# Performance work log

Hardware: AMD Instinct MI355X
Metric: run time of the kernel (lower is better)

The kernel has to match this reference:

```python
import jax, jax.numpy as jnp
import numpy as np

N = 100000
E = 1600000
F_IN = 128
HID = 64


def setup_inputs() -> dict:
    key = jax.random.key(0)
    ks = jax.random.split(key, 8)
    x = jax.random.normal(ks[0], (N, F_IN), dtype=jnp.float32)
    edge_index = jax.random.randint(ks[1], (2, E), 0, N, dtype=jnp.int32)
    # GCNConv params: weight [in, out] (glorot-ish scale), bias [out]
    W1 = jax.random.normal(ks[2], (F_IN, HID), dtype=jnp.float32) / np.sqrt(F_IN)
    b1 = jnp.zeros((HID,), dtype=jnp.float32)
    W2 = jax.random.normal(ks[3], (HID, HID), dtype=jnp.float32) / np.sqrt(HID)
    b2 = jnp.zeros((HID,), dtype=jnp.float32)
    Wc = jax.random.normal(ks[4], (HID, 1), dtype=jnp.float32) / np.sqrt(HID)
    bc = jnp.zeros((1,), dtype=jnp.float32)
    return {"x": x, "edge_index": edge_index, "W1": W1, "b1": b1,
            "W2": W2, "b2": b2, "Wc": Wc, "bc": bc}


def _gcn_conv(x, src, dst, W, b):
    # PyG GCNConv: h = x @ W, then symmetric-normalized aggregation over
    # edges with self-loops: out[d] = sum_e deg^-1/2[s] deg^-1/2[d] h[s] + b
    n = x.shape[0]
    h = x @ W                                            # [N, out]
    deg = jax.ops.segment_sum(jnp.ones_like(dst, dtype=h.dtype), dst,
                              num_segments=n)            # in-degree incl. self-loops
    dinv = jnp.where(deg > 0, jax.lax.rsqrt(deg), 0.0)   # [N]
    norm = dinv[src] * dinv[dst]                         # [E+N]
    msg = h[src] * norm[:, None]                         # gather + scale
    out = jax.ops.segment_sum(msg, dst, num_segments=n)  # scatter-add
    return out + b


def reference(x, edge_index, W1, b1, W2, b2, Wc, bc):
    n = x.shape[0]
    loop = jnp.arange(n, dtype=edge_index.dtype)
    src = jnp.concatenate([edge_index[0], loop])  # add self-loops
    dst = jnp.concatenate([edge_index[1], loop])
    h = jax.nn.relu(_gcn_conv(x, src, dst, W1, b1))  # dropout in eval mode = identity
    h = jax.nn.relu(_gcn_conv(h, src, dst, W2, b2))
    return (h @ Wc + bc).squeeze(-1)  # [N]
```

## Files before the change

kernel.cpp:

```cpp
#include <hip/hip_runtime.h>


#define FIN 128
#define HIDDEN 64
#define BUCK_SH 7
#define BUCK_MASK 127
#define NBUCK 782
#define CAP 2432
#define EPB 2048

typedef __attribute__((ext_vector_type(8))) short bf16x8;
typedef __attribute__((ext_vector_type(4))) float f32x4;

__device__ __forceinline__ unsigned f2bf_pair(float a, float b) {
    unsigned ua = __float_as_uint(a);
    unsigned ub = __float_as_uint(b);
    ua = (ua + 0x7FFFu + ((ua >> 16) & 1u)) >> 16;
    ub = (ub + 0x7FFFu + ((ub >> 16) & 1u)) & 0xFFFF0000u;
    return ua | ub;
}
__device__ __forceinline__ unsigned short f2bf1(float a) {
    unsigned u = __float_as_uint(a);
    return (unsigned short)((u + 0x7FFFu + ((u >> 16) & 1u)) >> 16);
}
#define BF_LO(u) __uint_as_float((u) << 16)
#define BF_HI(u) __uint_as_float((u) & 0xFFFF0000u)

__global__ __launch_bounds__(256) void k_prep(const float* __restrict__ w1,
                                              const float* __restrict__ w2,
                                              unsigned short* __restrict__ w1t,
                                              unsigned short* __restrict__ w2t,
                                              int* __restrict__ bcursor) {
    int t = blockIdx.x * 256 + threadIdx.x;
    if (t < NBUCK) bcursor[t] = 0;
    for (int i = t; i < 64 * FIN; i += 16384) {
        int ch = i >> 7, k = i & 127;
        w1t[i] = f2bf1(w1[k * 64 + ch]);
    }
    if (t < 64 * 64) {
        int ch = t >> 6, k = t & 63;
        w2t[t] = f2bf1(w2[k * 64 + ch]);
    }
}

__global__ __launch_bounds__(256) void k_scatter_mfma1(const int* __restrict__ src,
                                                       const int* __restrict__ dst,
                                                       int* __restrict__ bcursor,
                                                       int* __restrict__ pairs, int e,
                                                       const float4* __restrict__ x4,
                                                       const unsigned short* __restrict__ w1t,
                                                       uint2* __restrict__ hsb,
                                                       int n, int nsc, int ngm) {
    __shared__ int sbuf[4352];
    int tid = threadIdx.x;
    int bid = blockIdx.x;
    bool is_sc = (bid & 1) == 0;
    int id = bid >> 1;
    if (is_sc) {
        if (id >= nsc) return;
        int* h      = sbuf;
        int* base_s = sbuf + NBUCK;
        int* cur    = sbuf + 2 * NBUCK;
        int dloc[EPB / 256];
        for (int i = tid; i < NBUCK; i += 256) { h[i] = 0; cur[i] = 0; }
        __syncthreads();
        int start = id * EPB;
#pragma unroll
        for (int i = 0; i < EPB / 256; i++) {
            int idx = start + tid + i * 256;
            int d = (idx < e) ? dst[idx] : -1;
            dloc[i] = d;
            if (d >= 0) atomicAdd(&h[d >> BUCK_SH], 1);
        }
        __syncthreads();
        for (int i = tid; i < NBUCK; i += 256)
            if (h[i] > 0) base_s[i] = atomicAdd(&bcursor[i], h[i]);
        __syncthreads();
#pragma unroll
        for (int i = 0; i < EPB / 256; i++) {
            int idx = start + tid + i * 256;
            int d = dloc[i];
            if (d >= 0) {
                int b = d >> BUCK_SH;
                int pos = base_s[b] + atomicAdd(&cur[b], 1);
                if (pos < CAP) pairs[b * CAP + pos] = (src[idx] << BUCK_SH) | (d & BUCK_MASK);
            }
        }
        return;
    }
    if (id >= ngm) return;
    unsigned short* sW = (unsigned short*)sbuf;
    {
        int ch = tid >> 2, k0 = (tid & 3) * 32;
        const uint4* g = (const uint4*)(w1t + ch * 128 + k0);
        uint4* dsd = (uint4*)(sW + ch * 136 + k0);
        uint4 a = g[0], b = g[1], c = g[2], d = g[3];
        dsd[0] = a; dsd[1] = b; dsd[2] = c; dsd[3] = d;
    }
    __syncthreads();
    int lane = tid & 63, wave = tid >> 6;
    int quad = lane >> 4, nl = lane & 15;
    const bf16x8* sW8 = (const bf16x8*)sW;
    int node0g = id * 128;
#pragma unroll
    for (int hf = 0; hf < 2; hf++) {
        int node = node0g + hf * 64 + wave * 16 + nl;
        int ic = min(node, n - 1);
        const float4* px = x4 + (size_t)ic * 32 + quad * 2;
        bf16x8 bfr[4];
#pragma unroll
        for (int kc = 0; kc < 4; kc++) {
            float4 p = px[kc * 8];
            float4 q = px[kc * 8 + 1];
            union { unsigned u[4]; bf16x8 v; } t;
            t.u[0] = f2bf_pair(p.x, p.y); t.u[1] = f2bf_pair(p.z, p.w);
            t.u[2] = f2bf_pair(q.x, q.y); t.u[3] = f2bf_pair(q.z, q.w);
            bfr[kc] = t.v;
        }
        f32x4 a0 = {0.f, 0.f, 0.f, 0.f}, a1 = a0, a2 = a0, a3 = a0;
#pragma unroll
        for (int kc = 0; kc < 4; kc++) {
            int ko = kc * 4 + quad;
            bf16x8 w0  = sW8[(nl +  0) * 17 + ko];
            bf16x8 w1f = sW8[(nl + 16) * 17 + ko];
            bf16x8 w2f = sW8[(nl + 32) * 17 + ko];
            bf16x8 w3f = sW8[(nl + 48) * 17 + ko];
            a0 = __builtin_amdgcn_mfma_f32_16x16x32_bf16(w0,  bfr[kc], a0, 0, 0, 0);
            a1 = __builtin_amdgcn_mfma_f32_16x16x32_bf16(w1f, bfr[kc], a1, 0, 0, 0);
            a2 = __builtin_amdgcn_mfma_f32_16x16x32_bf16(w2f, bfr[kc], a2, 0, 0, 0);
            a3 = __builtin_amdgcn_mfma_f32_16x16x32_bf16(w3f, bfr[kc], a3, 0, 0, 0);
        }
        if (node < n) {
            uint2* o = hsb + (size_t)node * 16 + quad;
            o[0]  = make_uint2(f2bf_pair(a0.x, a0.y), f2bf_pair(a0.z, a0.w));
            o[4]  = make_uint2(f2bf_pair(a1.x, a1.y), f2bf_pair(a1.z, a1.w));
            o[8]  = make_uint2(f2bf_pair(a2.x, a2.y), f2bf_pair(a2.z, a2.w));
            o[12] = make_uint2(f2bf_pair(a3.x, a3.y), f2bf_pair(a3.z, a3.w));
        }
    }
}

__global__ __launch_bounds__(256) void k_count(const int* __restrict__ pairs,
                                               const int* __restrict__ bcursor,
                                               float* __restrict__ dinv, int n) {
    __shared__ int cnt[128];
    int tid = threadIdx.x, b = blockIdx.x;
    if (tid < 128) cnt[tid] = 0;
    __syncthreads();
    int c = min(bcursor[b], CAP);
    const int* pb = pairs + b * CAP;
    for (int i = tid; i < c; i += 256) atomicAdd(&cnt[pb[i] & BUCK_MASK], 1);
    __syncthreads();
    int node = (b << BUCK_SH) + tid;
    if (tid < 128 && node < n) dinv[node] = rsqrtf((float)cnt[tid] + 1.0f);
}

__global__ __launch_bounds__(256) void k_agg1_gemm2(const int* __restrict__ pairs,
                                                    const int* __restrict__ bcursor,
                                                    const float* __restrict__ dinv,
                                                    const uint4* __restrict__ hsb4,
                                                    const float4* __restrict__ b1_4,
                                                    const unsigned short* __restrict__ w2t,
                                                    uint2* __restrict__ hsb2, int n) {
    __shared__ int csr_l[CAP];
    __shared__ unsigned short sW[64 * 72];
    __shared__ float sV[32 * 68];
    __shared__ int cnt[128], off_s[128], wsum[128];
    int tid = threadIdx.x, b = blockIdx.x;
    int node0 = b << BUCK_SH;
    if (tid < 128) {
        int ch = tid >> 1, k0 = (tid & 1) * 32;
        const uint4* g = (const uint4*)(w2t + ch * 64 + k0);
        uint4* dsd = (uint4*)(sW + ch * 72 + k0);
        uint4 a = g[0], bb = g[1], c = g[2], d = g[3];
        dsd[0] = a; dsd[1] = bb; dsd[2] = c; dsd[3] = d;
    } else {
        cnt[tid - 128] = 0;
    }
    __syncthreads();
    int c = min(bcursor[b], CAP);
    const int* pb = pairs + b * CAP;
    for (int i = tid; i < c; i += 256) atomicAdd(&cnt[pb[i] & BUCK_MASK], 1);
    __syncthreads();
    if (tid < 128) wsum[tid] = cnt[tid];
    __syncthreads();
    for (int o = 1; o < 128; o <<= 1) {
        int x = 0;
        if (tid < 128 && tid >= o) x = wsum[tid - o];
        __syncthreads();
        if (tid < 128 && tid >= o) wsum[tid] += x;
        __syncthreads();
    }
    if (tid < 128) { off_s[tid] = wsum[tid] - cnt[tid]; cnt[tid] = 0; }
    __syncthreads();
    for (int i = tid; i < c; i += 256) {
        int p = pb[i];
        int l = p & BUCK_MASK;
        int pos = off_s[l] + atomicAdd(&cnt[l], 1);
        csr_l[pos] = p >> BUCK_SH;
    }
    __syncthreads();
    int nloc = tid >> 3, cq = tid & 7;
    int lane = tid & 63, wave = tid >> 6;
    int quad = lane >> 4, nl = lane & 15;
    const bf16x8* sW8 = (const bf16x8*)sW;
#pragma unroll 1
    for (int ck = 0; ck < 4; ck++) {
        int loc = ck * 32 + nloc;
        int node = node0 + loc;
        int dg = cnt[loc], st = off_s[loc];
        float sd = rsqrtf((float)dg + 1.0f);
        float4 accA = make_float4(0.f, 0.f, 0.f, 0.f), accB = accA;
        if (node < n) {
            int end = st + dg;
            int nr = (dg + 3) >> 2;
            for (int r = 0; r < nr; r++) {
                int base = st + (r << 2);
                int e0 = base, e1 = base + 1, e2 = base + 2, e3 = base + 3;
                int s0 = csr_l[min(e0, end - 1)];
                int s1 = csr_l[min(e1, end - 1)];
                int s2 = csr_l[min(e2, end - 1)];
                int s3 = csr_l[min(e3, end - 1)];
                float m0 = (e0 < end) ? dinv[s0] : 0.f;
                float m1 = (e1 < end) ? dinv[s1] : 0.f;
                float m2 = (e2 < end) ? dinv[s2] : 0.f;
                float m3 = (e3 < end) ? dinv[s3] : 0.f;
                uint4 g0 = hsb4[(size_t)s0 * 8 + cq];
                uint4 g1 = hsb4[(size_t)s1 * 8 + cq];
                uint4 g2 = hsb4[(size_t)s2 * 8 + cq];
                uint4 g3 = hsb4[(size_t)s3 * 8 + cq];
                accA.x += m0 * BF_LO(g0.x) + m1 * BF_LO(g1.x) + m2 * BF_LO(g2.x) + m3 * BF_LO(g3.x);
                accA.y += m0 * BF_HI(g0.x) + m1 * BF_HI(g1.x) + m2 * BF_HI(g2.x) + m3 * BF_HI(g3.x);
                accA.z += m0 * BF_LO(g0.y) + m1 * BF_LO(g1.y) + m2 * BF_LO(g2.y) + m3 * BF_LO(g3.y);
                accA.w += m0 * BF_HI(g0.y) + m1 * BF_HI(g1.y) + m2 * BF_HI(g2.y) + m3 * BF_HI(g3.y);
                accB.x += m0 * BF_LO(g0.z) + m1 * BF_LO(g1.z) + m2 * BF_LO(g2.z) + m3 * BF_LO(g3.z);
                accB.y += m0 * BF_HI(g0.z) + m1 * BF_HI(g1.z) + m2 * BF_HI(g2.z) + m3 * BF_HI(g3.z);
                accB.z += m0 * BF_LO(g0.w) + m1 * BF_LO(g1.w) + m2 * BF_LO(g2.w) + m3 * BF_LO(g3.w);
                accB.w += m0 * BF_HI(g0.w) + m1 * BF_HI(g1.w) + m2 * BF_HI(g2.w) + m3 * BF_HI(g3.w);
            }
        }
        float4 vA = make_float4(0.f, 0.f, 0.f, 0.f), vB = vA;
        if (node < n) {
            uint4 gs = hsb4[(size_t)node * 8 + cq];
            float sq = sd * sd;
            float4 bA = b1_4[cq * 2], bB = b1_4[cq * 2 + 1];
            vA.x = fmaxf(sd * accA.x + sq * BF_LO(gs.x) + bA.x, 0.f);
            vA.y = fmaxf(sd * accA.y + sq * BF_HI(gs.x) + bA.y, 0.f);
            vA.z = fmaxf(sd * accA.z + sq * BF_LO(gs.y) + bA.z, 0.f);
            vA.w = fmaxf(sd * accA.w + sq * BF_HI(gs.y) + bA.w, 0.f);
            vB.x = fmaxf(sd * accB.x + sq * BF_LO(gs.z) + bB.x, 0.f);
            vB.y = fmaxf(sd * accB.y + sq * BF_HI(gs.z) + bB.y, 0.f);
            vB.z = fmaxf(sd * accB.z + sq * BF_LO(gs.w) + bB.z, 0.f);
            vB.w = fmaxf(sd * accB.w + sq * BF_HI(gs.w) + bB.w, 0.f);
        }
        float* vb = sV + nloc * 68 + cq * 8;
        *(float4*)vb = vA;
        *(float4*)(vb + 4) = vB;
        __syncthreads();
#pragma unroll
        for (int tt = 0; tt < 2; tt++) {
            f32x4 acc = {0.f, 0.f, 0.f, 0.f};
#pragma unroll
            for (int kc = 0; kc < 2; kc++) {
                const float* vr = sV + (tt * 16 + nl) * 68 + kc * 32 + quad * 8;
                float4 p = *(const float4*)vr;
                float4 q = *(const float4*)(vr + 4);
                union { unsigned u[4]; bf16x8 v; } t;
                t.u[0] = f2bf_pair(p.x, p.y); t.u[1] = f2bf_pair(p.z, p.w);
                t.u[2] = f2bf_pair(q.x, q.y); t.u[3] = f2bf_pair(q.z, q.w);
                bf16x8 a = sW8[(wave * 16 + nl) * 9 + kc * 4 + quad];
                acc = __builtin_amdgcn_mfma_f32_16x16x32_bf16(a, t.v, acc, 0, 0, 0);
            }
            int oloc = ck * 32 + tt * 16 + nl;
            int onode = node0 + oloc;
            if (onode < n) {
                float s = rsqrtf((float)cnt[oloc] + 1.0f);
                hsb2[(size_t)onode * 16 + wave * 4 + quad] =
                    make_uint2(f2bf_pair(acc.x * s, acc.y * s), f2bf_pair(acc.z * s, acc.w * s));
            }
        }
        __syncthreads();
    }
}

__global__ __launch_bounds__(256) void k_agg2_head(const int* __restrict__ pairs,
                                                   const int* __restrict__ bcursor,
                                                   const uint4* __restrict__ hsb4,
                                                   const float4* __restrict__ b2_4,
                                                   const float4* __restrict__ wc_4,
                                                   const float* __restrict__ bc,
                                                   float* __restrict__ out, int n) {
    __shared__ int csr_l[CAP];
    __shared__ int cnt[128], off_s[128], wsum[128];
    int tid = threadIdx.x, b = blockIdx.x;
    int node0 = b << BUCK_SH;
    if (tid < 128) cnt[tid] = 0;
    __syncthreads();
    int c = min(bcursor[b], CAP);
    const int* pb = pairs + b * CAP;
    for (int i = tid; i < c; i += 256) atomicAdd(&cnt[pb[i] & BUCK_MASK], 1);
    __syncthreads();
    if (tid < 128) wsum[tid] = cnt[tid];
    __syncthreads();
    for (int o = 1; o < 128; o <<= 1) {
        int x = 0;
        if (tid < 128 && tid >= o) x = wsum[tid - o];
        __syncthreads();
        if (tid < 128 && tid >= o) wsum[tid] += x;
        __syncthreads();
    }
    if (tid < 128) { off_s[tid] = wsum[tid] - cnt[tid]; cnt[tid] = 0; }
    __syncthreads();
    for (int i = tid; i < c; i += 256) {
        int p = pb[i];
        int l = p & BUCK_MASK;
        int pos = off_s[l] + atomicAdd(&cnt[l], 1);
        csr_l[pos] = p >> BUCK_SH;
    }
    __syncthreads();
    int nloc = tid >> 3, cq = tid & 7;
#pragma unroll 1
    for (int ck = 0; ck < 4; ck++) {
        int loc = ck * 32 + nloc;
        int node = node0 + loc;
        if (node >= n) continue;
        int dg = cnt[loc], st = off_s[loc];
        int end = st + dg;
        float4 accA = make_float4(0.f, 0.f, 0.f, 0.f), accB = accA;
        int nr = (dg + 3) >> 2;
        for (int r = 0; r < nr; r++) {
            int base = st + (r << 2);
            int e0 = base, e1 = base + 1, e2 = base + 2, e3 = base + 3;
            int s0 = csr_l[min(e0, end - 1)];
            int s1 = csr_l[min(e1, end - 1)];
            int s2 = csr_l[min(e2, end - 1)];
            int s3 = csr_l[min(e3, end - 1)];
            float m0 = (e0 < end) ? 1.f : 0.f;
            float m1 = (e1 < end) ? 1.f : 0.f;
            float m2 = (e2 < end) ? 1.f : 0.f;
            float m3 = (e3 < end) ? 1.f : 0.f;
            uint4 g0 = hsb4[(size_t)s0 * 8 + cq];
            uint4 g1 = hsb4[(size_t)s1 * 8 + cq];
            uint4 g2 = hsb4[(size_t)s2 * 8 + cq];
            uint4 g3 = hsb4[(size_t)s3 * 8 + cq];
            accA.x += m0 * BF_LO(g0.x) + m1 * BF_LO(g1.x) + m2 * BF_LO(g2.x) + m3 * BF_LO(g3.x);
            accA.y += m0 * BF_HI(g0.x) + m1 * BF_HI(g1.x) + m2 * BF_HI(g2.x) + m3 * BF_HI(g3.x);
            accA.z += m0 * BF_LO(g0.y) + m1 * BF_LO(g1.y) + m2 * BF_LO(g2.y) + m3 * BF_LO(g3.y);
            accA.w += m0 * BF_HI(g0.y) + m1 * BF_HI(g1.y) + m2 * BF_HI(g2.y) + m3 * BF_HI(g3.y);
            accB.x += m0 * BF_LO(g0.z) + m1 * BF_LO(g1.z) + m2 * BF_LO(g2.z) + m3 * BF_LO(g3.z);
            accB.y += m0 * BF_HI(g0.z) + m1 * BF_HI(g1.z) + m2 * BF_HI(g2.z) + m3 * BF_HI(g3.z);
            accB.z += m0 * BF_LO(g0.w) + m1 * BF_LO(g1.w) + m2 * BF_LO(g2.w) + m3 * BF_LO(g3.w);
            accB.w += m0 * BF_HI(g0.w) + m1 * BF_HI(g1.w) + m2 * BF_HI(g2.w) + m3 * BF_HI(g3.w);
        }
        uint4 g = hsb4[(size_t)node * 8 + cq];
        float s = rsqrtf((float)dg + 1.0f);
        float4 bA = b2_4[cq * 2], bB = b2_4[cq * 2 + 1];
        float4 wA = wc_4[cq * 2], wB = wc_4[cq * 2 + 1];
        float t = fmaxf(s * (accA.x + BF_LO(g.x)) + bA.x, 0.f) * wA.x
                + fmaxf(s * (accA.y + BF_HI(g.x)) + bA.y, 0.f) * wA.y
                + fmaxf(s * (accA.z + BF_LO(g.y)) + bA.z, 0.f) * wA.z
                + fmaxf(s * (accA.w + BF_HI(g.y)) + bA.w, 0.f) * wA.w
                + fmaxf(s * (accB.x + BF_LO(g.z)) + bB.x, 0.f) * wB.x
                + fmaxf(s * (accB.y + BF_HI(g.z)) + bB.y, 0.f) * wB.y
                + fmaxf(s * (accB.z + BF_LO(g.w)) + bB.z, 0.f) * wB.z
                + fmaxf(s * (accB.w + BF_HI(g.w)) + bB.w, 0.f) * wB.w;
        t += __shfl_xor(t, 1);
        t += __shfl_xor(t, 2);
        t += __shfl_xor(t, 4);
        if (cq == 0) out[node] = t + bc[0];
    }
}

extern "C" void kernel_launch(void* const* d_in, const int* in_sizes, int n_in,
                              void* d_out, int out_size, void* d_ws, size_t ws_size,
                              hipStream_t stream) {
    const float* x  = (const float*)d_in[0];
    const int*   ei = (const int*)d_in[1];
    const float* W1 = (const float*)d_in[2];
    const float* b1 = (const float*)d_in[3];
    const float* W2 = (const float*)d_in[4];
    const float* b2 = (const float*)d_in[5];
    const float* Wc = (const float*)d_in[6];
    const float* bc = (const float*)d_in[7];
    int n = in_sizes[0] / FIN;
    int e = in_sizes[1] / 2;
    const int* srcv = ei;
    const int* dstv = ei + e;

    char* ws = (char*)d_ws;
    float* dinv    = (float*)(ws + 0);
    int*   bcursor = (int*)(ws + (512u << 10));
    unsigned short* w1t = (unsigned short*)(ws + (528u << 10));
    unsigned short* w2t = (unsigned short*)(ws + (548u << 10));
    int*   pairs   = (int*)(ws + (1u << 20));
    uint2* hsb1    = (uint2*)(ws + (9u << 20));
    uint2* hsb2    = (uint2*)(ws + (22u << 20));

    int nb_sc   = (e + EPB - 1) / EPB;
    int nb_rows = (n + 127) / 128;
    int nb_max  = max(nb_sc, nb_rows);

    k_prep<<<64, 256, 0, stream>>>(W1, W2, w1t, w2t, bcursor);
    k_scatter_mfma1<<<2 * nb_max, 256, 0, stream>>>(srcv, dstv, bcursor, pairs, e,
                                                    (const float4*)x, w1t, hsb1,
                                                    n, nb_sc, nb_rows);
    k_count<<<NBUCK, 256, 0, stream>>>(pairs, bcursor, dinv, n);
    k_agg1_gemm2<<<NBUCK, 256, 0, stream>>>(pairs, bcursor, dinv, (const uint4*)hsb1,
                                            (const float4*)b1, w2t, hsb2, n);
    k_agg2_head<<<NBUCK, 256, 0, stream>>>(pairs, bcursor, (const uint4*)hsb2,
                                           (const float4*)b2, (const float4*)Wc,
                                           bc, (float*)d_out, n);
}
```

Before: 218.2 us.

## Interleave two nodes per gather loop and retile scatter/GEMM block layout

The aggregation loops in both layer kernels now handle two destination nodes per thread group at once, issuing eight independent gathers per iteration instead of four. The goal is more memory-level parallelism on the latency-bound random gathers. The scatter kernel now handles twice as many edges per block, and its scatter and GEMM blocks are laid out contiguously rather than interleaved by parity, which removes idle early-exit blocks. The cost is higher register pressure, wasted work when the two paired nodes have uneven degrees, and padding writes to csr_l so out-of-range reads stay safe.

Result: faster. 212.1 us (-2.8%).

```diff
diff --git a/kernel.cpp b/kernel.cpp
--- a/kernel.cpp
+++ b/kernel.cpp
@@ -7,7 +7,7 @@
 #define BUCK_MASK 127
 #define NBUCK 782
 #define CAP 2432
-#define EPB 2048
+#define EPB 4096
 
 typedef __attribute__((ext_vector_type(8))) short bf16x8;
 typedef __attribute__((ext_vector_type(4))) float f32x4;
@@ -50,14 +50,12 @@
                                                        const float4* __restrict__ x4,
                                                        const unsigned short* __restrict__ w1t,
                                                        uint2* __restrict__ hsb,
-                                                       int n, int nsc, int ngm) {
+                                                       int n, int nsc) {
     __shared__ int sbuf[4352];
     int tid = threadIdx.x;
     int bid = blockIdx.x;
-    bool is_sc = (bid & 1) == 0;
-    int id = bid >> 1;
-    if (is_sc) {
-        if (id >= nsc) return;
+    if (bid < nsc) {
+        int id = bid;
         int* h      = sbuf;
         int* base_s = sbuf + NBUCK;
         int* cur    = sbuf + 2 * NBUCK;
@@ -88,7 +86,7 @@
         }
         return;
     }
-    if (id >= ngm) return;
+    int id = bid - nsc;
     unsigned short* sW = (unsigned short*)sbuf;
     {
         int ch = tid >> 2, k0 = (tid & 3) * 32;
@@ -172,8 +170,8 @@
         int ch = tid >> 1, k0 = (tid & 1) * 32;
         const uint4* g = (const uint4*)(w2t + ch * 64 + k0);
         uint4* dsd = (uint4*)(sW + ch * 72 + k0);
-        uint4 a = g[0], bb = g[1], c = g[2], d = g[3];
-        dsd[0] = a; dsd[1] = bb; dsd[2] = c; dsd[3] = d;
+        uint4 a = g[0], bb = g[1], c2 = g[2], d = g[3];
+        dsd[0] = a; dsd[1] = bb; dsd[2] = c2; dsd[3] = d;
     } else {
         cnt[tid - 128] = 0;
     }
@@ -199,87 +197,99 @@
         int pos = off_s[l] + atomicAdd(&cnt[l], 1);
         csr_l[pos] = p >> BUCK_SH;
     }
+    if (c + tid < CAP) csr_l[c + tid] = 0;
     __syncthreads();
     int nloc = tid >> 3, cq = tid & 7;
     int lane = tid & 63, wave = tid >> 6;
     int quad = lane >> 4, nl = lane & 15;
     const bf16x8* sW8 = (const bf16x8*)sW;
 #pragma unroll 1
-    for (int ck = 0; ck < 4; ck++) {
-        int loc = ck * 32 + nloc;
-        int node = node0 + loc;
-        int dg = cnt[loc], st = off_s[loc];
-        float sd = rsqrtf((float)dg + 1.0f);
-        float4 accA = make_float4(0.f, 0.f, 0.f, 0.f), accB = accA;
-        if (node < n) {
-            int end = st + dg;
-            int nr = (dg + 3) >> 2;
-            for (int r = 0; r < nr; r++) {
-                int base = st + (r << 2);
-                int e0 = base, e1 = base + 1, e2 = base + 2, e3 = base + 3;
-                int s0 = csr_l[min(e0, end - 1)];
-                int s1 = csr_l[min(e1, end - 1)];
-                int s2 = csr_l[min(e2, end - 1)];
-                int s3 = csr_l[min(e3, end - 1)];
-                float m0 = (e0 < end) ? dinv[s0] : 0.f;
-                float m1 = (e1 < end) ? dinv[s1] : 0.f;
-                float m2 = (e2 < end) ? dinv[s2] : 0.f;
-                float m3 = (e3 < end) ? dinv[s3] : 0.f;
-                uint4 g0 = hsb4[(size_t)s0 * 8 + cq];
-                uint4 g1 = hsb4[(size_t)s1 * 8 + cq];
-                uint4 g2 = hsb4[(size_t)s2 * 8 + cq];
-                uint4 g3 = hsb4[(size_t)s3 * 8 + cq];
-                accA.x += m0 * BF_LO(g0.x) + m1 * BF_LO(g1.x) + m2 * BF_LO(g2.x) + m3 * BF_LO(g3.x);
-                accA.y += m0 * BF_HI(g0.x) + m1 * BF_HI(g1.x) + m2 * BF_HI(g2.x) + m3 * BF_HI(g3.x);
-                accA.z += m0 * BF_LO(g0.y) + m1 * BF_LO(g1.y) + m2 * BF_LO(g2.y) + m3 * BF_LO(g3.y);
-                accA.w += m0 * BF_HI(g0.y) + m1 * BF_HI(g1.y) + m2 * BF_HI(g2.y) + m3 * BF_HI(g3.y);
-                accB.x += m0 * BF_LO(g0.z) + m1 * BF_LO(g1.z) + m2 * BF_LO(g2.z) + m3 * BF_LO(g3.z);
-                accB.y += m0 * BF_HI(g0.z) + m1 * BF_HI(g1.z) + m2 * BF_HI(g2.z) + m3 * BF_HI(g3.z);
-                accB.z += m0 * BF_LO(g0.w) + m1 * BF_LO(g1.w) + m2 * BF_LO(g2.w) + m3 * BF_LO(g3.w);
-                accB.w += m0 * BF_HI(g0.w) + m1 * BF_HI(g1.w) + m2 * BF_HI(g2.w) + m3 * BF_HI(g3.w);
+    for (int pk = 0; pk < 2; pk++) {
+        int locA = pk * 64 + nloc, locB = locA + 32;
+        int dgA = cnt[locA], stA = off_s[locA], endA = stA + dgA;
+        int dgB = cnt[locB], stB = off_s[locB], endB = stB + dgB;
+        float4 aAA = make_float4(0.f, 0.f, 0.f, 0.f), aAB = aAA;
+        float4 aBA = aAA, aBB = aAA;
+        int nr = max((dgA + 3) >> 2, (dgB + 3) >> 2);
+        for (int r = 0; r < nr; r++) {
+            int bA = stA + (r << 2), bB = stB + (r << 2);
+            int sA[4], sB[4];
+            float mA[4], mB[4];
+            uint4 gA[4], gB[4];
+#pragma unroll
+            for (int j = 0; j < 4; j++) sA[j] = csr_l[max(min(bA + j, endA - 1), 0)];
+#pragma unroll
+            for (int j = 0; j < 4; j++) sB[j] = csr_l[max(min(bB + j, endB - 1), 0)];
+#pragma unroll
+            for (int j = 0; j < 4; j++) mA[j] = (bA + j < endA) ? dinv[sA[j]] : 0.f;
+#pragma unroll
+            for (int j = 0; j < 4; j++) mB[j] = (bB + j < endB) ? dinv[sB[j]] : 0.f;
+#pragma unroll
+            for (int j = 0; j < 4; j++) gA[j] = hsb4[(size_t)sA[j] * 8 + cq];
+#pragma unroll
+            for (int j = 0; j < 4; j++) gB[j] = hsb4[(size_t)sB[j] * 8 + cq];
+#pragma unroll
+            for (int j = 0; j < 4; j++) {
+                aAA.x += mA[j] * BF_LO(gA[j].x); aAA.y += mA[j] * BF_HI(gA[j].x);
+                aAA.z += mA[j] * BF_LO(gA[j].y); aAA.w += mA[j] * BF_HI(gA[j].y);
+                aAB.x += mA[j] * BF_LO(gA[j].z); aAB.y += mA[j] * BF_HI(gA[j].z);
+                aAB.z += mA[j] * BF_LO(gA[j].w); aAB.w += mA[j] * BF_HI(gA[j].w);
+                aBA.x += mB[j] * BF_LO(gB[j].x); aBA.y += mB[j] * BF_HI(gB[j].x);
+                aBA.z += mB[j] * BF_LO(gB[j].y); aBA.w += mB[j] * BF_HI(gB[j].y);
+                aBB.x += mB[j] * BF_LO(gB[j].z); aBB.y += mB[j] * BF_HI(gB[j].z);
+                aBB.z += mB[j] * BF_LO(gB[j].w); aBB.w += mB[j] * BF_HI(gB[j].w);
             }
         }
-        float4 vA = make_float4(0.f, 0.f, 0.f, 0.f), vB = vA;
-        if (node < n) {
-            uint4 gs = hsb4[(size_t)node * 8 + cq];
-            float sq = sd * sd;
-            float4 bA = b1_4[cq * 2], bB = b1_4[cq * 2 + 1];
-            vA.x = fmaxf(sd * accA.x + sq * BF_LO(gs.x) + bA.x, 0.f);
-            vA.y = fmaxf(sd * accA.y + sq * BF_HI(gs.x) + bA.y, 0.f);
-            vA.z = fmaxf(sd * accA.z + sq * BF_LO(gs.y) + bA.z, 0.f);
-            vA.w = fmaxf(sd * accA.w + sq * BF_HI(gs.y) + bA.w, 0.f);
-            vB.x = fmaxf(sd * accB.x + sq * BF_LO(gs.z) + bB.x, 0.f);
-            vB.y = fmaxf(sd * accB.y + sq * BF_HI(gs.z) + bB.y, 0.f);
-            vB.z = fmaxf(sd * accB.z + sq * BF_LO(gs.w) + bB.z, 0.f);
-            vB.w = fmaxf(sd * accB.w + sq * BF_HI(gs.w) + bB.w, 0.f);
-        }
-        float* vb = sV + nloc * 68 + cq * 8;
-        *(float4*)vb = vA;
-        *(float4*)(vb + 4) = vB;
-        __syncthreads();
-#pragma unroll
-        for (int tt = 0; tt < 2; tt++) {
-            f32x4 acc = {0.f, 0.f, 0.f, 0.f};
-#pragma unroll
-            for (int kc = 0; kc < 2; kc++) {
-                const float* vr = sV + (tt * 16 + nl) * 68 + kc * 32 + quad * 8;
-                float4 p = *(const float4*)vr;
-                float4 q = *(const float4*)(vr + 4);
-                union { unsigned u[4]; bf16x8 v; } t;
-                t.u[0] = f2bf_pair(p.x, p.y); t.u[1] = f2bf_pair(p.z, p.w);
-                t.u[2] = f2bf_pair(q.x, q.y); t.u[3] = f2bf_pair(q.z, q.w);
-                bf16x8 a = sW8[(wave * 16 + nl) * 9 + kc * 4 + quad];
-                acc = __builtin_amdgcn_mfma_f32_16x16x32_bf16(a, t.v, acc, 0, 0, 0);
+#pragma unroll
+        for (int sub = 0; sub < 2; sub++) {
+            int loc = pk * 64 + sub * 32 + nloc;
+            int node = node0 + loc;
+            float4 xA = sub ? aBA : aAA;
+            float4 xB = sub ? aBB : aAB;
+            int dg = sub ? dgB : dgA;
+            float4 vA = make_float4(0.f, 0.f, 0.f, 0.f), vB = vA;
+            if (node < n) {
+                float sd = rsqrtf((float)dg + 1.0f);
+                float sq = sd * sd;
+                uint4 gs = hsb4[(size_t)node * 8 + cq];
+                float4 bA = b1_4[cq * 2], bB = b1_4[cq * 2 + 1];
+                vA.x = fmaxf(sd * xA.x + sq * BF_LO(gs.x) + bA.x, 0.f);
+                vA.y = fmaxf(sd * xA.y + sq * BF_HI(gs.x) + bA.y, 0.f);
+                vA.z = fmaxf(sd * xA.z + sq * BF_LO(gs.y) + bA.z, 0.f);
+                vA.w = fmaxf(sd * xA.w + sq * BF_HI(gs.y) + bA.w, 0.f);
+                vB.x = fmaxf(sd * xB.x + sq * BF_LO(gs.z) + bB.x, 0.f);
+                vB.y = fmaxf(sd * xB.y + sq * BF_HI(gs.z) + bB.y, 0.f);
+                vB.z = fmaxf(sd * xB.z + sq * BF_LO(gs.w) + bB.z, 0.f);
+                vB.w = fmaxf(sd * xB.w + sq * BF_HI(gs.w) + bB.w, 0.f);
             }
-            int oloc = ck * 32 + tt * 16 + nl;
-            int onode = node0 + oloc;
-            if (onode < n) {
-                float s = rsqrtf((float)cnt[oloc] + 1.0f);
-                hsb2[(size_t)onode * 16 + wave * 4 + quad] =
-                    make_uint2(f2bf_pair(acc.x * s, acc.y * s), f2bf_pair(acc.z * s, acc.w * s));
+            float* vb = sV + nloc * 68 + cq * 8;
+            *(float4*)vb = vA;
+            *(float4*)(vb + 4) = vB;
+            __syncthreads();
+#pragma unroll
+            for (int tt = 0; tt < 2; tt++) {
+                f32x4 acc = {0.f, 0.f, 0.f, 0.f};
+#pragma unroll
+                for (int kc = 0; kc < 2; kc++) {
+                    const float* vr = sV + (tt * 16 + nl) * 68 + kc * 32 + quad * 8;
+                    float4 p = *(const float4*)vr;
+                    float4 q = *(const float4*)(vr + 4);
+                    union { unsigned u[4]; bf16x8 v; } t;
+                    t.u[0] = f2bf_pair(p.x, p.y); t.u[1] = f2bf_pair(p.z, p.w);
+                    t.u[2] = f2bf_pair(q.x, q.y); t.u[3] = f2bf_pair(q.z, q.w);
+                    bf16x8 a = sW8[(wave * 16 + nl) * 9 + kc * 4 + quad];
+                    acc = __builtin_amdgcn_mfma_f32_16x16x32_bf16(a, t.v, acc, 0, 0, 0);
+                }
+                int oloc = pk * 64 + sub * 32 + tt * 16 + nl;
+                int onode = node0 + oloc;
+                if (onode < n) {
+                    float s = rsqrtf((float)cnt[oloc] + 1.0f);
+                    hsb2[(size_t)onode * 16 + wave * 4 + quad] =
+                        make_uint2(f2bf_pair(acc.x * s, acc.y * s), f2bf_pair(acc.z * s, acc.w * s));
+                }
             }
-        }
-        __syncthreads();
+            __syncthreads();
+        }
     }
 }
 
@@ -317,57 +327,71 @@
         int pos = off_s[l] + atomicAdd(&cnt[l], 1);
         csr_l[pos] = p >> BUCK_SH;
     }
+    if (c + tid < CAP) csr_l[c + tid] = 0;
     __syncthreads();
     int nloc = tid >> 3, cq = tid & 7;
 #pragma unroll 1
-    for (int ck = 0; ck < 4; ck++) {
-        int loc = ck * 32 + nloc;
-        int node = node0 + loc;
-        if (node >= n) continue;
-        int dg = cnt[loc], st = off_s[loc];
-        int end = st + dg;
-        float4 accA = make_float4(0.f, 0.f, 0.f, 0.f), accB = accA;
-        int nr = (dg + 3) >> 2;
+    for (int pk = 0; pk < 2; pk++) {
+        int locA = pk * 64 + nloc, locB = locA + 32;
+        int dgA = cnt[locA], stA = off_s[locA], endA = stA + dgA;
+        int dgB = cnt[locB], stB = off_s[locB], endB = stB + dgB;
+        float4 aAA = make_float4(0.f, 0.f, 0.f, 0.f), aAB = aAA;
+        float4 aBA = aAA, aBB = aAA;
+        int nr = max((dgA + 3) >> 2, (dgB + 3) >> 2);
         for (int r = 0; r < nr; r++) {
-            int base = st + (r << 2);
-            int e0 = base, e1 = base + 1, e2 = base + 2, e3 = base + 3;
-            int s0 = csr_l[min(e0, end - 1)];
-            int s1 = csr_l[min(e1, end - 1)];
-            int s2 = csr_l[min(e2, end - 1)];
-            int s3 = csr_l[min(e3, end - 1)];
-            float m0 = (e0 < end) ? 1.f : 0.f;
-            float m1 = (e1 < end) ? 1.f : 0.f;
-            float m2 = (e2 < end) ? 1.f : 0.f;
-            float m3 = (e3 < end) ? 1.f : 0.f;
-            uint4 g0 = hsb4[(size_t)s0 * 8 + cq];
-            uint4 g1 = hsb4[(size_t)s1 * 8 + cq];
-            uint4 g2 = hsb4[(size_t)s2 * 8 + cq];
-            uint4 g3 = hsb4[(size_t)s3 * 8 + cq];
-            accA.x += m0 * BF_LO(g0.x) + m1 * BF_LO(g1.x) + m2 * BF_LO(g2.x) + m3 * BF_LO(g3.x);
-            accA.y += m0 * BF_HI(g0.x) + m1 * BF_HI(g1.x) + m2 * BF_HI(g2.x) + m3 * BF_HI(g3.x);
-            accA.z += m0 * BF_LO(g0.y) + m1 * BF_LO(g1.y) + m2 * BF_LO(g2.y) + m3 * BF_LO(g3.y);
-            accA.w += m0 * BF_HI(g0.y) + m1 * BF_HI(g1.y) + m2 * BF_HI(g2.y) + m3 * BF_HI(g3.y);
-            accB.x += m0 * BF_LO(g0.z) + m1 * BF_LO(g1.z) + m2 * BF_LO(g2.z) + m3 * BF_LO(g3.z);
-            accB.y += m0 * BF_HI(g0.z) + m1 * BF_HI(g1.z) + m2 * BF_HI(g2.z) + m3 * BF_HI(g3.z);
-            accB.z += m0 * BF_LO(g0.w) + m1 * BF_LO(g1.w) + m2 * BF_LO(g2.w) + m3 * BF_LO(g3.w);
-            accB.w += m0 * BF_HI(g0.w) + m1 * BF_HI(g1.w) + m2 * BF_HI(g2.w) + m3 * BF_HI(g3.w);
-        }
-        uint4 g = hsb4[(size_t)node * 8 + cq];
-        float s = rsqrtf((float)dg + 1.0f);
-        float4 bA = b2_4[cq * 2], bB = b2_4[cq * 2 + 1];
-        float4 wA = wc_4[cq * 2], wB = wc_4[cq * 2 + 1];
-        float t = fmaxf(s * (accA.x + BF_LO(g.x)) + bA.x, 0.f) * wA.x
-                + fmaxf(s * (accA.y + BF_HI(g.x)) + bA.y, 0.f) * wA.y
-                + fmaxf(s * (accA.z + BF_LO(g.y)) + bA.z, 0.f) * wA.z
-                + fmaxf(s * (accA.w + BF_HI(g.y)) + bA.w, 0.f) * wA.w
-                + fmaxf(s * (accB.x + BF_LO(g.z)) + bB.x, 0.f) * wB.x
-                + fmaxf(s * (accB.y + BF_HI(g.z)) + bB.y, 0.f) * wB.y
-                + fmaxf(s * (accB.z + BF_LO(g.w)) + bB.z, 0.f) * wB.z
-                + fmaxf(s * (accB.w + BF_HI(g.w)) + bB.w, 0.f) * wB.w;
-        t += __shfl_xor(t, 1);
-        t += __shfl_xor(t, 2);
-        t += __shfl_xor(t, 4);
-        if (cq == 0) out[node] = t + bc[0];
+            int bA = stA + (r << 2), bB = stB + (r << 2);
+            int sA[4], sB[4];
+            float mA[4], mB[4];
+            uint4 gA[4], gB[4];
+#pragma unroll
+            for (int j = 0; j < 4; j++) sA[j] = csr_l[max(min(bA + j, endA - 1), 0)];
+#pragma unroll
+            for (int j = 0; j < 4; j++) sB[j] = csr_l[max(min(bB + j, endB - 1), 0)];
+#pragma unroll
+            for (int j = 0; j < 4; j++) mA[j] = (bA + j < endA) ? 1.f : 0.f;
+#pragma unroll
+            for (int j = 0; j < 4; j++) mB[j] = (bB + j < endB) ? 1.f : 0.f;
+#pragma unroll
+            for (int j = 0; j < 4; j++) gA[j] = hsb4[(size_t)sA[j] * 8 + cq];
+#pragma unroll
+            for (int j = 0; j < 4; j++) gB[j] = hsb4[(size_t)sB[j] * 8 + cq];
+#pragma unroll
+            for (int j = 0; j < 4; j++) {
+                aAA.x += mA[j] * BF_LO(gA[j].x); aAA.y += mA[j] * BF_HI(gA[j].x);
+                aAA.z += mA[j] * BF_LO(gA[j].y); aAA.w += mA[j] * BF_HI(gA[j].y);
+                aAB.x += mA[j] * BF_LO(gA[j].z); aAB.y += mA[j] * BF_HI(gA[j].z);
+                aAB.z += mA[j] * BF_LO(gA[j].w); aAB.w += mA[j] * BF_HI(gA[j].w);
+                aBA.x += mB[j] * BF_LO(gB[j].x); aBA.y += mB[j] * BF_HI(gB[j].x);
+                aBA.z += mB[j] * BF_LO(gB[j].y); aBA.w += mB[j] * BF_HI(gB[j].y);
+                aBB.x += mB[j] * BF_LO(gB[j].z); aBB.y += mB[j] * BF_HI(gB[j].z);
+                aBB.z += mB[j] * BF_LO(gB[j].w); aBB.w += mB[j] * BF_HI(gB[j].w);
+            }
+        }
+#pragma unroll
+        for (int sub = 0; sub < 2; sub++) {
+            int loc = pk * 64 + sub * 32 + nloc;
+            int node = node0 + loc;
+            if (node >= n) continue;
+            float4 xA = sub ? aBA : aAA;
+            float4 xB = sub ? aBB : aAB;
+            int dg = sub ? dgB : dgA;
+            uint4 g = hsb4[(size_t)node * 8 + cq];
+            float s = rsqrtf((float)dg + 1.0f);
+            float4 bA = b2_4[cq * 2], bB = b2_4[cq * 2 + 1];
+            float4 wA = wc_4[cq * 2], wB = wc_4[cq * 2 + 1];
+            float t = fmaxf(s * (xA.x + BF_LO(g.x)) + bA.x, 0.f) * wA.x
+                    + fmaxf(s * (xA.y + BF_HI(g.x)) + bA.y, 0.f) * wA.y
+                    + fmaxf(s * (xA.z + BF_LO(g.y)) + bA.z, 0.f) * wA.z
+                    + fmaxf(s * (xA.w + BF_HI(g.y)) + bA.w, 0.f) * wA.w
+                    + fmaxf(s * (xB.x + BF_LO(g.z)) + bB.x, 0.f) * wB.x
+                    + fmaxf(s * (xB.y + BF_HI(g.z)) + bB.y, 0.f) * wB.y
+                    + fmaxf(s * (xB.z + BF_LO(g.w)) + bB.z, 0.f) * wB.z
+                    + fmaxf(s * (xB.w + BF_HI(g.w)) + bB.w, 0.f) * wB.w;
+            t += __shfl_xor(t, 1);
+            t += __shfl_xor(t, 2);
+            t += __shfl_xor(t, 4);
+            if (cq == 0) out[node] = t + bc[0];
+        }
     }
 }
 
@@ -398,12 +422,11 @@
 
     int nb_sc   = (e + EPB - 1) / EPB;
     int nb_rows = (n + 127) / 128;
-    int nb_max  = max(nb_sc, nb_rows);
 
     k_prep<<<64, 256, 0, stream>>>(W1, W2, w1t, w2t, bcursor);
-    k_scatter_mfma1<<<2 * nb_max, 256, 0, stream>>>(srcv, dstv, bcursor, pairs, e,
-                                                    (const float4*)x, w1t, hsb1,
-                                                    n, nb_sc, nb_rows);
+    k_scatter_mfma1<<<nb_sc + nb_rows, 256, 0, stream>>>(srcv, dstv, bcursor, pairs, e,
+                                                         (const float4*)x, w1t, hsb1,
+                                                         n, nb_sc);
     k_count<<<NBUCK, 256, 0, stream>>>(pairs, bcursor, dinv, n);
     k_agg1_gemm2<<<NBUCK, 256, 0, stream>>>(pairs, bcursor, dinv, (const uint4*)hsb1,
                                             (const float4*)b1, w2t, hsb2, n);
```
